# Kernel tuning notes

Hardware: AMD Instinct MI355X
Metric: run time of the kernel (lower is better)

Reference implementation:

```python
import jax, jax.numpy as jnp
import numpy as np
from jax import lax

B, T, H = 32768, 64, 16
VOCAB_USER = 600001
VOCAB_LAUNCH = 3


def setup_inputs() -> dict:
    key = jax.random.key(0)
    ks = jax.random.split(key, 10)
    s = 1.0 / np.sqrt(H)
    return {
        "user_id": jax.random.randint(ks[0], (B,), 0, VOCAB_USER),
        "launch_seq": jax.random.randint(ks[1], (B, T), 0, VOCAB_LAUNCH),
        "user_emb": jax.random.normal(ks[2], (VOCAB_USER, H), dtype=jnp.float32),
        "launch_emb": jax.random.normal(ks[3], (VOCAB_LAUNCH, H), dtype=jnp.float32),
        "W_ih": jax.random.uniform(ks[4], (3 * H, H), jnp.float32, -s, s),
        "W_hh": jax.random.uniform(ks[5], (3 * H, H), jnp.float32, -s, s),
        "b_ih": jax.random.uniform(ks[6], (3 * H,), jnp.float32, -s, s),
        "b_hh": jax.random.uniform(ks[7], (3 * H,), jnp.float32, -s, s),
        "fc_W": jax.random.uniform(ks[8], (1, 2 * H), jnp.float32, -s, s),
        "fc_b": jax.random.uniform(ks[9], (1,), jnp.float32, -s, s),
    }


def reference(user_id, launch_seq, user_emb, launch_emb, W_ih, W_hh, b_ih, b_hh, fc_W, fc_b):
    u = user_emb[user_id]                      # (B, H)
    x = launch_emb[launch_seq]                 # (B, T, H)
    # precompute input contributions to the gates for all timesteps
    gx_all = jnp.einsum('bth,gh->btg', x, W_ih) + b_ih  # (B, T, 3H)

    def step(h, gx):
        gh = h @ W_hh.T + b_hh                 # (B, 3H)
        r = jax.nn.sigmoid(gx[:, :H] + gh[:, :H])
        z = jax.nn.sigmoid(gx[:, H:2 * H] + gh[:, H:2 * H])
        n = jnp.tanh(gx[:, 2 * H:] + r * gh[:, 2 * H:])
        h_new = (1.0 - z) * n + z * h
        return h_new, h_new

    h0 = jnp.zeros((x.shape[0], H), dtype=x.dtype)
    _, hs = lax.scan(step, h0, jnp.swapaxes(gx_all, 0, 1))  # hs: (T, B, H)
    pooled = jnp.mean(hs, axis=0)              # (B, H)
    fc_in = jnp.concatenate([u, pooled], axis=1)  # (B, 2H)
    return fc_in @ fc_W.T + fc_b               # (B, 1)
```

## Files before the change

### kernel.cpp

```cpp
#include <hip/hip_runtime.h>
#include <hip/hip_bf16.h>
#include <string.h>


#define NBLK 1024

typedef __attribute__((ext_vector_type(8)))  short    short8;
typedef __attribute__((ext_vector_type(16))) float    floatx16;
typedef __attribute__((ext_vector_type(4)))  unsigned uintx4;

static __device__ __forceinline__ float fexp2(float x) { return __builtin_amdgcn_exp2f(x); }
static __device__ __forceinline__ float frcp(float x)  { return __builtin_amdgcn_rcpf(x); }
static __device__ __forceinline__ unsigned f2u(float f) { unsigned u; memcpy(&u, &f, 4); return u; }
static __device__ __forceinline__ unsigned short bfrne(float f) {
    union { __hip_bfloat16 b; unsigned short u; } cv; cv.b = __float2bfloat16(f); return cv.u;
}
static __device__ __forceinline__ float bf2f(unsigned short u) {
    unsigned v = ((unsigned)u) << 16; float f; memcpy(&f, &v, 4); return f;
}
static __device__ __forceinline__ unsigned pkrnd(float a, float b) {
    unsigned ua = f2u(a) + 0x8000u;
    unsigned ub = f2u(b) + 0x8000u;
    return __builtin_amdgcn_perm(ub, ua, 0x07060302u);
}
static __device__ __forceinline__ float sel3f(int c, float a0, float a1, float a2) {
    return c == 0 ? a0 : (c == 1 ? a1 : a2);
}
static __device__ __forceinline__ unsigned sel3u(int c, unsigned a0, unsigned a1, unsigned a2) {
    return c == 0 ? a0 : (c == 1 ? a1 : a2);
}

__global__ __launch_bounds__(64) void gru_mfma32(
    const int* __restrict__ user_id,
    const int* __restrict__ launch_seq,
    const float* __restrict__ user_emb,
    const float* __restrict__ launch_emb,
    const float* __restrict__ W_ih,
    const float* __restrict__ W_hh,
    const float* __restrict__ b_ih,
    const float* __restrict__ b_hh,
    const float* __restrict__ fc_W,
    const float* __restrict__ fc_b,
    float* __restrict__ out)
{
    constexpr float L  = 1.4426950408889634f;
    constexpr float L2 = 2.8853900817779268f;

    __shared__ float gxlut[144];

    const int tid  = threadIdx.x;
    const int n    = tid & 31;
    const int half = tid >> 5;
    const int d1o  = 4 * half;
    const long long sampBase = (long long)blockIdx.x * 32;

    unsigned pk[4];
    {
        const int* sp = launch_seq + (sampBase + n) * 64;
        #pragma unroll
        for (int w = 0; w < 4; ++w) {
            unsigned p = 0;
            #pragma unroll
            for (int j = 0; j < 4; ++j) {
                int4 v = ((const int4*)sp)[w * 4 + j];
                p |= ((unsigned)v.x & 3u) << (2 * (4 * j + 0));
                p |= ((unsigned)v.y & 3u) << (2 * (4 * j + 1));
                p |= ((unsigned)v.z & 3u) << (2 * (4 * j + 2));
                p |= ((unsigned)v.w & 3u) << (2 * (4 * j + 3));
            }
            pk[w] = p;
        }
    }

    for (int idx = tid; idx < 144; idx += 64) {
        int s = idx / 48, g = idx - s * 48;
        float dot = b_ih[g];
        #pragma unroll
        for (int k = 0; k < 16; ++k)
            dot = fmaf(W_ih[g * 16 + k], launch_emb[s * 16 + k], dot);
        int gate = g >> 4, dim = g & 15;
        gxlut[(gate * 3 + s) * 16 + dim] =
            (g < 32) ? (-L * (dot + b_hh[g])) : (L2 * dot);
    }

    short8 Arz, An;
    {
        auto pack8 = [&](const float* w) {
            uintx4 hi;
            #pragma unroll
            for (int p = 0; p < 4; ++p)
                hi[p] = (unsigned)bfrne(w[2 * p]) | ((unsigned)bfrne(w[2 * p + 1]) << 16);
            return __builtin_bit_cast(short8, hi);
        };
        float w[8];
        const float* rowrz = W_hh + n * 16;
        float4 a = *(const float4*)(rowrz + d1o);
        float4 b = *(const float4*)(rowrz + d1o + 8);
        w[0] = -L * a.x; w[1] = -L * a.y; w[2] = -L * a.z; w[3] = -L * a.w;
        w[4] = -L * b.x; w[5] = -L * b.y; w[6] = -L * b.z; w[7] = -L * b.w;
        Arz = pack8(w);
        if (n < 16) {
            const float* rown = W_hh + (32 + n) * 16;
            a = *(const float4*)(rown + d1o);
            b = *(const float4*)(rown + d1o + 8);
            w[0] = L2 * a.x; w[1] = L2 * a.y; w[2] = L2 * a.z; w[3] = L2 * a.w;
            w[4] = L2 * b.x; w[5] = L2 * b.y; w[6] = L2 * b.z; w[7] = L2 * b.w;
        } else {
            #pragma unroll
            for (int j = 0; j < 8; ++j) w[j] = 0.f;
        }
        An = pack8(w);
    }

    __syncthreads();

    short8 Agx;
    {
        uintx4 d = {0u, 0u, 0u, 0u};
        if (half == 0) {
            const float* base = (n < 16) ? &gxlut[0] : &gxlut[48];
            int dim = n & 15;
            float g0 = base[0 * 16 + dim];
            float g1 = base[1 * 16 + dim];
            float g2 = base[2 * 16 + dim];
            unsigned short h0 = bfrne(g0), h1 = bfrne(g1), h2 = bfrne(g2);
            d[0] = (unsigned)h0 | ((unsigned)h1 << 16);
            d[1] = (unsigned)h2 | ((unsigned)bfrne(g0 - bf2f(h0)) << 16);
            d[2] = (unsigned)bfrne(g1 - bf2f(h1)) | ((unsigned)bfrne(g2 - bf2f(h2)) << 16);
        }
        Agx = __builtin_bit_cast(short8, d);
    }

    const unsigned khA = half ? 0u : 0x3F80u;
    const unsigned khB = half ? 0u : 0x3F800000u;

    floatx16 Cn;
    #pragma unroll
    for (int i = 0; i < 16; ++i) Cn[i] = 0.f;
    {
        float4 a = *(const float4*)&b_hh[32 + d1o];
        float4 b = *(const float4*)&b_hh[32 + d1o + 8];
        Cn[0] = L2 * a.x; Cn[1] = L2 * a.y; Cn[2] = L2 * a.z; Cn[3] = L2 * a.w;
        Cn[4] = L2 * b.x; Cn[5] = L2 * b.y; Cn[6] = L2 * b.z; Cn[7] = L2 * b.w;
    }

    float gxn[3][8];
    #pragma unroll
    for (int c = 0; c < 3; ++c) {
        float4 a = *(const float4*)&gxlut[(6 + c) * 16 + d1o];
        float4 b = *(const float4*)&gxlut[(6 + c) * 16 + d1o + 8];
        gxn[c][0] = a.x; gxn[c][1] = a.y; gxn[c][2] = a.z; gxn[c][3] = a.w;
        gxn[c][4] = b.x; gxn[c][5] = b.y; gxn[c][6] = b.z; gxn[c][7] = b.w;
    }

    floatx16 CZ;
    #pragma unroll
    for (int i = 0; i < 16; ++i) CZ[i] = 0.f;

    float h[8], pool[8];
    #pragma unroll
    for (int j = 0; j < 8; ++j) { h[j] = 0.f; pool[j] = 0.f; }
    short8 B = {0, 0, 0, 0, 0, 0, 0, 0};

    short8 Bp;
    {
        int c0 = (int)(pk[0] & 3u);
        uintx4 bp = { sel3u(c0, khA, khB, 0u),
                      sel3u(c0, khB, 0u, khA),
                      sel3u(c0, 0u, khA, khB), 0u };
        Bp = __builtin_bit_cast(short8, bp);
    }

    #pragma unroll
    for (int w = 0; w < 4; ++w) {
        unsigned cw  = pk[w];
        unsigned ncw = (pk[w] >> 2) | (w < 3 ? (pk[w + 1] << 30) : 0u);
        #pragma unroll
        for (int tt = 0; tt < 16; ++tt) {
            int c = (int)(cw & 3u);

            floatx16 t1  = __builtin_amdgcn_mfma_f32_32x32x16_bf16(Agx, Bp, CZ, 0, 0, 0);
            floatx16 dn  = __builtin_amdgcn_mfma_f32_32x32x16_bf16(An,  B, Cn, 0, 0, 0);
            floatx16 drz = __builtin_amdgcn_mfma_f32_32x32x16_bf16(Arz, B, t1, 0, 0, 0);

            #pragma unroll
            for (int j = 0; j < 8; ++j) {
                float gn = sel3f(c, gxn[0][j], gxn[1][j], gxn[2][j]);
                float r  = frcp(1.0f + fexp2(drz[j]));
                float z  = frcp(1.0f + fexp2(drz[8 + j]));
                float y  = fmaf(r, dn[j], gn);
                float nn = fmaf(-2.0f, frcp(1.0f + fexp2(y)), 1.0f);
                h[j] = fmaf(z, h[j] - nn, nn);
                pool[j] += h[j];
            }

            int cn = (int)(ncw & 3u);
            uintx4 bp = { sel3u(cn, khA, khB, 0u),
                          sel3u(cn, khB, 0u, khA),
                          sel3u(cn, 0u, khA, khB), 0u };
            Bp = __builtin_bit_cast(short8, bp);
            uintx4 b;
            b[0] = pkrnd(h[0], h[1]);
            b[1] = pkrnd(h[2], h[3]);
            b[2] = pkrnd(h[4], h[5]);
            b[3] = pkrnd(h[6], h[7]);
            B = __builtin_bit_cast(short8, b);
            cw >>= 2;
            ncw >>= 2;
        }
    }

    float4 f1a = *(const float4*)&fc_W[d1o];
    float4 f1b = *(const float4*)&fc_W[d1o + 8];
    float4 f2a = *(const float4*)&fc_W[16 + d1o];
    float4 f2b = *(const float4*)&fc_W[16 + d1o + 8];
    int uid = user_id[sampBase + n];
    float4 ua = *(const float4*)&user_emb[(long long)uid * 16 + d1o];
    float4 ub = *(const float4*)&user_emb[(long long)uid * 16 + d1o + 8];
    const float inv64 = 1.0f / 64.0f;
    float val = f1a.x * ua.x + f1a.y * ua.y + f1a.z * ua.z + f1a.w * ua.w
              + f1b.x * ub.x + f1b.y * ub.y + f1b.z * ub.z + f1b.w * ub.w;
    val = fmaf(f2a.x * inv64, pool[0], val);
    val = fmaf(f2a.y * inv64, pool[1], val);
    val = fmaf(f2a.z * inv64, pool[2], val);
    val = fmaf(f2a.w * inv64, pool[3], val);
    val = fmaf(f2b.x * inv64, pool[4], val);
    val = fmaf(f2b.y * inv64, pool[5], val);
    val = fmaf(f2b.z * inv64, pool[6], val);
    val = fmaf(f2b.w * inv64, pool[7], val);
    val += __shfl_xor(val, 32);
    if (half == 0) out[sampBase + n] = val + fc_b[0];
}

extern "C" void kernel_launch(void* const* d_in, const int* in_sizes, int n_in,
                              void* d_out, int out_size, void* d_ws, size_t ws_size,
                              hipStream_t stream) {
    const int*   user_id    = (const int*)d_in[0];
    const int*   launch_seq = (const int*)d_in[1];
    const float* user_emb   = (const float*)d_in[2];
    const float* launch_emb = (const float*)d_in[3];
    const float* W_ih       = (const float*)d_in[4];
    const float* W_hh       = (const float*)d_in[5];
    const float* b_ih       = (const float*)d_in[6];
    const float* b_hh       = (const float*)d_in[7];
    const float* fc_W       = (const float*)d_in[8];
    const float* fc_b       = (const float*)d_in[9];
    float* out = (float*)d_out;

    gru_mfma32<<<dim3(NBLK), dim3(64), 0, stream>>>(
        user_id, launch_seq, user_emb, launch_emb,
        W_ih, W_hh, b_ih, b_hh, fc_W, fc_b, out);
}
```

Before: 126.6 us.

## Split GRU gate math across two cooperating waves with LDS hidden-state exchange

Each block now runs two wavefronts for the same 32 samples. Both waves issue the full MFMAs redundantly, but each computes the gate nonlinearities for only half of the hidden dimensions. The halves of the hidden state are exchanged through double-buffered shared memory with a barrier every timestep, and a final cross-wave reduction produces the output. The aim is to halve the serial transcendental work per wave on the recurrence critical path, at the cost of duplicated MFMAs, a block barrier per step, and a partial loop unroll.

```diff
diff --git a/kernel.cpp b/kernel.cpp
--- a/kernel.cpp
+++ b/kernel.cpp
@@ -30,7 +30,7 @@
     return c == 0 ? a0 : (c == 1 ? a1 : a2);
 }
 
-__global__ __launch_bounds__(64) void gru_mfma32(
+__global__ __launch_bounds__(128) void gru_coop(
     const int* __restrict__ user_id,
     const int* __restrict__ launch_seq,
     const float* __restrict__ user_emb,
@@ -46,12 +46,17 @@
     constexpr float L  = 1.4426950408889634f;
     constexpr float L2 = 2.8853900817779268f;
 
-    __shared__ float gxlut[144];
+    __shared__ float    gxlut[144];
+    __shared__ unsigned xch[2][2][64][2];
+    __shared__ float    redc[2][32];
 
     const int tid  = threadIdx.x;
-    const int n    = tid & 31;
-    const int half = tid >> 5;
+    const int wid  = tid >> 6;
+    const int lane = tid & 63;
+    const int n    = lane & 31;
+    const int half = lane >> 5;
     const int d1o  = 4 * half;
+    const int dimo = d1o + 8 * wid;
     const long long sampBase = (long long)blockIdx.x * 32;
 
     unsigned pk[4];
@@ -72,7 +77,7 @@
         }
     }
 
-    for (int idx = tid; idx < 144; idx += 64) {
+    for (int idx = tid; idx < 144; idx += 128) {
         int s = idx / 48, g = idx - s * 48;
         float dot = b_ih[g];
         #pragma unroll
@@ -144,22 +149,21 @@
         Cn[4] = L2 * b.x; Cn[5] = L2 * b.y; Cn[6] = L2 * b.z; Cn[7] = L2 * b.w;
     }
 
-    float gxn[3][8];
-    #pragma unroll
-    for (int c = 0; c < 3; ++c) {
-        float4 a = *(const float4*)&gxlut[(6 + c) * 16 + d1o];
-        float4 b = *(const float4*)&gxlut[(6 + c) * 16 + d1o + 8];
-        gxn[c][0] = a.x; gxn[c][1] = a.y; gxn[c][2] = a.z; gxn[c][3] = a.w;
-        gxn[c][4] = b.x; gxn[c][5] = b.y; gxn[c][6] = b.z; gxn[c][7] = b.w;
+    float gxn0[4], gxn1[4], gxn2[4];
+    #pragma unroll
+    for (int jj = 0; jj < 4; ++jj) {
+        gxn0[jj] = gxlut[(6 + 0) * 16 + dimo + jj];
+        gxn1[jj] = gxlut[(6 + 1) * 16 + dimo + jj];
+        gxn2[jj] = gxlut[(6 + 2) * 16 + dimo + jj];
     }
 
     floatx16 CZ;
     #pragma unroll
     for (int i = 0; i < 16; ++i) CZ[i] = 0.f;
 
-    float h[8], pool[8];
-    #pragma unroll
-    for (int j = 0; j < 8; ++j) { h[j] = 0.f; pool[j] = 0.f; }
+    float h4[4], pool4[4];
+    #pragma unroll
+    for (int jj = 0; jj < 4; ++jj) { h4[jj] = 0.f; pool4[jj] = 0.f; }
     short8 B = {0, 0, 0, 0, 0, 0, 0, 0};
 
     short8 Bp;
@@ -175,7 +179,7 @@
     for (int w = 0; w < 4; ++w) {
         unsigned cw  = pk[w];
         unsigned ncw = (pk[w] >> 2) | (w < 3 ? (pk[w + 1] << 30) : 0u);
-        #pragma unroll
+        #pragma unroll 2
         for (int tt = 0; tt < 16; ++tt) {
             int c = (int)(cw & 3u);
 
@@ -183,53 +187,61 @@
             floatx16 dn  = __builtin_amdgcn_mfma_f32_32x32x16_bf16(An,  B, Cn, 0, 0, 0);
             floatx16 drz = __builtin_amdgcn_mfma_f32_32x32x16_bf16(Arz, B, t1, 0, 0, 0);
 
-            #pragma unroll
-            for (int j = 0; j < 8; ++j) {
-                float gn = sel3f(c, gxn[0][j], gxn[1][j], gxn[2][j]);
-                float r  = frcp(1.0f + fexp2(drz[j]));
-                float z  = frcp(1.0f + fexp2(drz[8 + j]));
-                float y  = fmaf(r, dn[j], gn);
-                float nn = fmaf(-2.0f, frcp(1.0f + fexp2(y)), 1.0f);
-                h[j] = fmaf(z, h[j] - nn, nn);
-                pool[j] += h[j];
-            }
-
-            int cn = (int)(ncw & 3u);
-            uintx4 bp = { sel3u(cn, khA, khB, 0u),
-                          sel3u(cn, khB, 0u, khA),
-                          sel3u(cn, 0u, khA, khB), 0u };
+            auto gates = [&](int JO) {
+                #pragma unroll
+                for (int jj = 0; jj < 4; ++jj) {
+                    float gn = sel3f(c, gxn0[jj], gxn1[jj], gxn2[jj]);
+                    float r  = frcp(1.0f + fexp2(drz[JO + jj]));
+                    float z  = frcp(1.0f + fexp2(drz[8 + JO + jj]));
+                    float y  = fmaf(r, dn[JO + jj], gn);
+                    float nn = fmaf(-2.0f, frcp(1.0f + fexp2(y)), 1.0f);
+                    h4[jj] = fmaf(z, h4[jj] - nn, nn);
+                    pool4[jj] += h4[jj];
+                }
+            };
+            if (wid == 0) gates(0); else gates(4);
+
+            unsigned hp0 = pkrnd(h4[0], h4[1]);
+            unsigned hp1 = pkrnd(h4[2], h4[3]);
+            int buf = tt & 1;
+            xch[buf][wid][lane][0] = hp0;
+            xch[buf][wid][lane][1] = hp1;
+            __syncthreads();
+            unsigned tw0 = xch[buf][wid ^ 1][lane][0];
+            unsigned tw1 = xch[buf][wid ^ 1][lane][1];
+
+            uintx4 b;
+            b[0] = wid ? tw0 : hp0;
+            b[1] = wid ? tw1 : hp1;
+            b[2] = wid ? hp0 : tw0;
+            b[3] = wid ? hp1 : tw1;
+            B = __builtin_bit_cast(short8, b);
+
+            int cnx = (int)(ncw & 3u);
+            uintx4 bp = { sel3u(cnx, khA, khB, 0u),
+                          sel3u(cnx, khB, 0u, khA),
+                          sel3u(cnx, 0u, khA, khB), 0u };
             Bp = __builtin_bit_cast(short8, bp);
-            uintx4 b;
-            b[0] = pkrnd(h[0], h[1]);
-            b[1] = pkrnd(h[2], h[3]);
-            b[2] = pkrnd(h[4], h[5]);
-            b[3] = pkrnd(h[6], h[7]);
-            B = __builtin_bit_cast(short8, b);
             cw >>= 2;
             ncw >>= 2;
         }
     }
 
-    float4 f1a = *(const float4*)&fc_W[d1o];
-    float4 f1b = *(const float4*)&fc_W[d1o + 8];
-    float4 f2a = *(const float4*)&fc_W[16 + d1o];
-    float4 f2b = *(const float4*)&fc_W[16 + d1o + 8];
+    float4 f1 = *(const float4*)&fc_W[dimo];
+    float4 f2 = *(const float4*)&fc_W[16 + dimo];
     int uid = user_id[sampBase + n];
-    float4 ua = *(const float4*)&user_emb[(long long)uid * 16 + d1o];
-    float4 ub = *(const float4*)&user_emb[(long long)uid * 16 + d1o + 8];
+    float4 uu = *(const float4*)&user_emb[(long long)uid * 16 + dimo];
     const float inv64 = 1.0f / 64.0f;
-    float val = f1a.x * ua.x + f1a.y * ua.y + f1a.z * ua.z + f1a.w * ua.w
-              + f1b.x * ub.x + f1b.y * ub.y + f1b.z * ub.z + f1b.w * ub.w;
-    val = fmaf(f2a.x * inv64, pool[0], val);
-    val = fmaf(f2a.y * inv64, pool[1], val);
-    val = fmaf(f2a.z * inv64, pool[2], val);
-    val = fmaf(f2a.w * inv64, pool[3], val);
-    val = fmaf(f2b.x * inv64, pool[4], val);
-    val = fmaf(f2b.y * inv64, pool[5], val);
-    val = fmaf(f2b.z * inv64, pool[6], val);
-    val = fmaf(f2b.w * inv64, pool[7], val);
+    float val = f1.x * uu.x + f1.y * uu.y + f1.z * uu.z + f1.w * uu.w;
+    val = fmaf(f2.x * inv64, pool4[0], val);
+    val = fmaf(f2.y * inv64, pool4[1], val);
+    val = fmaf(f2.z * inv64, pool4[2], val);
+    val = fmaf(f2.w * inv64, pool4[3], val);
     val += __shfl_xor(val, 32);
-    if (half == 0) out[sampBase + n] = val + fc_b[0];
+    if (half == 0) redc[wid][n] = val;
+    __syncthreads();
+    if (wid == 0 && half == 0)
+        out[sampBase + n] = redc[0][n] + redc[1][n] + fc_b[0];
 }
 
 extern "C" void kernel_launch(void* const* d_in, const int* in_sizes, int n_in,
@@ -247,7 +259,7 @@
     const float* fc_b       = (const float*)d_in[9];
     float* out = (float*)d_out;
 
-    gru_mfma32<<<dim3(NBLK), dim3(64), 0, stream>>>(
+    gru_coop<<<dim3(NBLK), dim3(128), 0, stream>>>(
         user_id, launch_seq, user_emb, launch_emb,
         W_ih, W_hh, b_ih, b_hh, fc_W, fc_b, out);
 }
```

After: 233.6 us. 1.85x slower.

## Switch GRU recurrence to 16x16x32 MFMA with 16 samples per wave

Applied to the files above, without the earlier changes.

Restructures the recurrent step to use three 16x16x32 bf16 MFMAs (r, z, n gates), with 16 samples per 64-lane wave instead of 32, doubling the block count. The input-gate lookup and biases are folded into an extra K-slice (quad 2) of the B operand via one-hot rows, and the hidden state is redistributed across lanes with ds_bpermute each step. The sigmoid pair shares one reciprocal. The aim is a shorter per-step MFMA latency chain and more waves to hide it, at the cost of per-step cross-lane permutes and less work per wave.

```diff
diff --git a/kernel.cpp b/kernel.cpp
--- a/kernel.cpp
+++ b/kernel.cpp
@@ -3,11 +3,11 @@
 #include <string.h>
 
 
-#define NBLK 1024
-
-typedef __attribute__((ext_vector_type(8)))  short    short8;
-typedef __attribute__((ext_vector_type(16))) float    floatx16;
-typedef __attribute__((ext_vector_type(4)))  unsigned uintx4;
+#define NBLK 2048
+
+typedef __attribute__((ext_vector_type(8))) short    short8;
+typedef __attribute__((ext_vector_type(4))) float    floatx4;
+typedef __attribute__((ext_vector_type(4))) unsigned uintx4;
 
 static __device__ __forceinline__ float fexp2(float x) { return __builtin_amdgcn_exp2f(x); }
 static __device__ __forceinline__ float frcp(float x)  { return __builtin_amdgcn_rcpf(x); }
@@ -30,7 +30,7 @@
     return c == 0 ? a0 : (c == 1 ? a1 : a2);
 }
 
-__global__ __launch_bounds__(64) void gru_mfma32(
+__global__ __launch_bounds__(64) void gru16(
     const int* __restrict__ user_id,
     const int* __restrict__ launch_seq,
     const float* __restrict__ user_emb,
@@ -45,18 +45,20 @@
 {
     constexpr float L  = 1.4426950408889634f;
     constexpr float L2 = 2.8853900817779268f;
+    constexpr unsigned K_LO = 0x3F80u;
+    constexpr unsigned K_HI = 0x3F800000u;
 
     __shared__ float gxlut[144];
 
     const int tid  = threadIdx.x;
-    const int n    = tid & 31;
-    const int half = tid >> 5;
-    const int d1o  = 4 * half;
-    const long long sampBase = (long long)blockIdx.x * 32;
+    const int col  = tid & 15;
+    const int quad = tid >> 4;
+    const bool isq2 = (quad == 2);
+    const long long sampBase = (long long)blockIdx.x * 16;
 
     unsigned pk[4];
     {
-        const int* sp = launch_seq + (sampBase + n) * 64;
+        const int* sp = launch_seq + (sampBase + col) * 64;
         #pragma unroll
         for (int w = 0; w < 4; ++w) {
             unsigned p = 0;
@@ -83,7 +85,9 @@
             (g < 32) ? (-L * (dot + b_hh[g])) : (L2 * dot);
     }
 
-    short8 Arz, An;
+    __syncthreads();
+
+    short8 Ar, Az, An_;
     {
         auto pack8 = [&](const float* w) {
             uintx4 hi;
@@ -92,144 +96,122 @@
                 hi[p] = (unsigned)bfrne(w[2 * p]) | ((unsigned)bfrne(w[2 * p + 1]) << 16);
             return __builtin_bit_cast(short8, hi);
         };
-        float w[8];
-        const float* rowrz = W_hh + n * 16;
-        float4 a = *(const float4*)(rowrz + d1o);
-        float4 b = *(const float4*)(rowrz + d1o + 8);
-        w[0] = -L * a.x; w[1] = -L * a.y; w[2] = -L * a.z; w[3] = -L * a.w;
-        w[4] = -L * b.x; w[5] = -L * b.y; w[6] = -L * b.z; w[7] = -L * b.w;
-        Arz = pack8(w);
-        if (n < 16) {
-            const float* rown = W_hh + (32 + n) * 16;
-            a = *(const float4*)(rown + d1o);
-            b = *(const float4*)(rown + d1o + 8);
-            w[0] = L2 * a.x; w[1] = L2 * a.y; w[2] = L2 * a.z; w[3] = L2 * a.w;
-            w[4] = L2 * b.x; w[5] = L2 * b.y; w[6] = L2 * b.z; w[7] = L2 * b.w;
-        } else {
+        auto makeA = [&](int grow, float scale, const float* gx3, float bias, short8& A) {
+            float w[8];
             #pragma unroll
             for (int j = 0; j < 8; ++j) w[j] = 0.f;
-        }
-        An = pack8(w);
-    }
-
-    __syncthreads();
-
-    short8 Agx;
-    {
-        uintx4 d = {0u, 0u, 0u, 0u};
-        if (half == 0) {
-            const float* base = (n < 16) ? &gxlut[0] : &gxlut[48];
-            int dim = n & 15;
-            float g0 = base[0 * 16 + dim];
-            float g1 = base[1 * 16 + dim];
-            float g2 = base[2 * 16 + dim];
-            unsigned short h0 = bfrne(g0), h1 = bfrne(g1), h2 = bfrne(g2);
-            d[0] = (unsigned)h0 | ((unsigned)h1 << 16);
-            d[1] = (unsigned)h2 | ((unsigned)bfrne(g0 - bf2f(h0)) << 16);
-            d[2] = (unsigned)bfrne(g1 - bf2f(h1)) | ((unsigned)bfrne(g2 - bf2f(h2)) << 16);
-        }
-        Agx = __builtin_bit_cast(short8, d);
-    }
-
-    const unsigned khA = half ? 0u : 0x3F80u;
-    const unsigned khB = half ? 0u : 0x3F800000u;
-
-    floatx16 Cn;
-    #pragma unroll
-    for (int i = 0; i < 16; ++i) Cn[i] = 0.f;
-    {
-        float4 a = *(const float4*)&b_hh[32 + d1o];
-        float4 b = *(const float4*)&b_hh[32 + d1o + 8];
-        Cn[0] = L2 * a.x; Cn[1] = L2 * a.y; Cn[2] = L2 * a.z; Cn[3] = L2 * a.w;
-        Cn[4] = L2 * b.x; Cn[5] = L2 * b.y; Cn[6] = L2 * b.z; Cn[7] = L2 * b.w;
-    }
-
-    float gxn[3][8];
-    #pragma unroll
-    for (int c = 0; c < 3; ++c) {
-        float4 a = *(const float4*)&gxlut[(6 + c) * 16 + d1o];
-        float4 b = *(const float4*)&gxlut[(6 + c) * 16 + d1o + 8];
-        gxn[c][0] = a.x; gxn[c][1] = a.y; gxn[c][2] = a.z; gxn[c][3] = a.w;
-        gxn[c][4] = b.x; gxn[c][5] = b.y; gxn[c][6] = b.z; gxn[c][7] = b.w;
-    }
-
-    floatx16 CZ;
-    #pragma unroll
-    for (int i = 0; i < 16; ++i) CZ[i] = 0.f;
-
-    float h[8], pool[8];
-    #pragma unroll
-    for (int j = 0; j < 8; ++j) { h[j] = 0.f; pool[j] = 0.f; }
-    short8 B = {0, 0, 0, 0, 0, 0, 0, 0};
-
-    short8 Bp;
+            if (quad < 2) {
+                const float* row = W_hh + (grow + col) * 16 + quad * 8;
+                float4 a = *(const float4*)row;
+                float4 b = *(const float4*)(row + 4);
+                w[0] = scale * a.x; w[1] = scale * a.y; w[2] = scale * a.z; w[3] = scale * a.w;
+                w[4] = scale * b.x; w[5] = scale * b.y; w[6] = scale * b.z; w[7] = scale * b.w;
+            } else if (quad == 2) {
+                if (gx3) {
+                    #pragma unroll
+                    for (int c = 0; c < 3; ++c) {
+                        float g = gx3[c * 16 + col];
+                        w[c] = g;
+                        w[3 + c] = g - bf2f(bfrne(g));
+                    }
+                } else {
+                    w[6] = bias;
+                    w[7] = bias - bf2f(bfrne(bias));
+                }
+            }
+            A = pack8(w);
+        };
+        makeA(0,  -L, &gxlut[0],       0.f,               Ar);
+        makeA(16, -L, &gxlut[3 * 16],  0.f,               Az);
+        makeA(32,  L2, (const float*)0, L2 * b_hh[32 + col], An_);
+    }
+
+    floatx4 gn0 = *(const floatx4*)&gxlut[(6 + 0) * 16 + quad * 4];
+    floatx4 gn1 = *(const floatx4*)&gxlut[(6 + 1) * 16 + quad * 4];
+    floatx4 gn2 = *(const floatx4*)&gxlut[(6 + 2) * 16 + quad * 4];
+
+    const int a_lo = (col + 32 * (quad & 1)) * 4;
+    const int a_hi = a_lo + 64;
+
+    floatx4 h    = {0.f, 0.f, 0.f, 0.f};
+    floatx4 pool = {0.f, 0.f, 0.f, 0.f};
+    const floatx4 CZ = {0.f, 0.f, 0.f, 0.f};
+
+    short8 B;
     {
         int c0 = (int)(pk[0] & 3u);
-        uintx4 bp = { sel3u(c0, khA, khB, 0u),
-                      sel3u(c0, khB, 0u, khA),
-                      sel3u(c0, 0u, khA, khB), 0u };
-        Bp = __builtin_bit_cast(short8, bp);
+        uintx4 b = {0u, 0u, 0u, 0u};
+        if (isq2) {
+            b[0] = sel3u(c0, K_LO, K_HI, 0u);
+            b[1] = sel3u(c0, K_HI, 0u, K_LO);
+            b[2] = sel3u(c0, 0u, K_LO, K_HI);
+            b[3] = K_LO | K_HI;
+        }
+        B = __builtin_bit_cast(short8, b);
     }
 
     #pragma unroll
     for (int w = 0; w < 4; ++w) {
         unsigned cw  = pk[w];
         unsigned ncw = (pk[w] >> 2) | (w < 3 ? (pk[w + 1] << 30) : 0u);
-        #pragma unroll
+        #pragma unroll 4
         for (int tt = 0; tt < 16; ++tt) {
             int c = (int)(cw & 3u);
 
-            floatx16 t1  = __builtin_amdgcn_mfma_f32_32x32x16_bf16(Agx, Bp, CZ, 0, 0, 0);
-            floatx16 dn  = __builtin_amdgcn_mfma_f32_32x32x16_bf16(An,  B, Cn, 0, 0, 0);
-            floatx16 drz = __builtin_amdgcn_mfma_f32_32x32x16_bf16(Arz, B, t1, 0, 0, 0);
-
-            #pragma unroll
-            for (int j = 0; j < 8; ++j) {
-                float gn = sel3f(c, gxn[0][j], gxn[1][j], gxn[2][j]);
-                float r  = frcp(1.0f + fexp2(drz[j]));
-                float z  = frcp(1.0f + fexp2(drz[8 + j]));
-                float y  = fmaf(r, dn[j], gn);
+            floatx4 dr = __builtin_amdgcn_mfma_f32_16x16x32_bf16(Ar,  B, CZ, 0, 0, 0);
+            floatx4 dz = __builtin_amdgcn_mfma_f32_16x16x32_bf16(Az,  B, CZ, 0, 0, 0);
+            floatx4 dn = __builtin_amdgcn_mfma_f32_16x16x32_bf16(An_, B, CZ, 0, 0, 0);
+
+            #pragma unroll
+            for (int e = 0; e < 4; ++e) {
+                float er = fexp2(dr[e]);
+                float ez = fexp2(dz[e]);
+                float t1 = 1.0f + er;
+                float t2 = 1.0f + ez;
+                float rp = frcp(t1 * t2);
+                float r  = rp * t2;
+                float z  = rp * t1;
+                float gn = sel3f(c, gn0[e], gn1[e], gn2[e]);
+                float y  = fmaf(r, dn[e], gn);
                 float nn = fmaf(-2.0f, frcp(1.0f + fexp2(y)), 1.0f);
-                h[j] = fmaf(z, h[j] - nn, nn);
-                pool[j] += h[j];
+                h[e] = fmaf(z, h[e] - nn, nn);
+                pool[e] += h[e];
             }
 
+            unsigned hp0 = pkrnd(h[0], h[1]);
+            unsigned hp1 = pkrnd(h[2], h[3]);
             int cn = (int)(ncw & 3u);
-            uintx4 bp = { sel3u(cn, khA, khB, 0u),
-                          sel3u(cn, khB, 0u, khA),
-                          sel3u(cn, 0u, khA, khB), 0u };
-            Bp = __builtin_bit_cast(short8, bp);
             uintx4 b;
-            b[0] = pkrnd(h[0], h[1]);
-            b[1] = pkrnd(h[2], h[3]);
-            b[2] = pkrnd(h[4], h[5]);
-            b[3] = pkrnd(h[6], h[7]);
+            b[0] = (unsigned)__builtin_amdgcn_ds_bpermute(a_lo, (int)hp0);
+            b[1] = (unsigned)__builtin_amdgcn_ds_bpermute(a_lo, (int)hp1);
+            b[2] = (unsigned)__builtin_amdgcn_ds_bpermute(a_hi, (int)hp0);
+            b[3] = (unsigned)__builtin_amdgcn_ds_bpermute(a_hi, (int)hp1);
+            unsigned oh0 = sel3u(cn, K_LO, K_HI, 0u);
+            unsigned oh1 = sel3u(cn, K_HI, 0u, K_LO);
+            unsigned oh2 = sel3u(cn, 0u, K_LO, K_HI);
+            b[0] = isq2 ? oh0 : b[0];
+            b[1] = isq2 ? oh1 : b[1];
+            b[2] = isq2 ? oh2 : b[2];
+            b[3] = isq2 ? (K_LO | K_HI) : b[3];
             B = __builtin_bit_cast(short8, b);
             cw >>= 2;
             ncw >>= 2;
         }
     }
 
-    float4 f1a = *(const float4*)&fc_W[d1o];
-    float4 f1b = *(const float4*)&fc_W[d1o + 8];
-    float4 f2a = *(const float4*)&fc_W[16 + d1o];
-    float4 f2b = *(const float4*)&fc_W[16 + d1o + 8];
-    int uid = user_id[sampBase + n];
-    float4 ua = *(const float4*)&user_emb[(long long)uid * 16 + d1o];
-    float4 ub = *(const float4*)&user_emb[(long long)uid * 16 + d1o + 8];
+    float4 f1 = *(const float4*)&fc_W[quad * 4];
+    float4 f2 = *(const float4*)&fc_W[16 + quad * 4];
+    int uid = user_id[sampBase + col];
+    float4 uu = *(const float4*)&user_emb[(long long)uid * 16 + quad * 4];
     const float inv64 = 1.0f / 64.0f;
-    float val = f1a.x * ua.x + f1a.y * ua.y + f1a.z * ua.z + f1a.w * ua.w
-              + f1b.x * ub.x + f1b.y * ub.y + f1b.z * ub.z + f1b.w * ub.w;
-    val = fmaf(f2a.x * inv64, pool[0], val);
-    val = fmaf(f2a.y * inv64, pool[1], val);
-    val = fmaf(f2a.z * inv64, pool[2], val);
-    val = fmaf(f2a.w * inv64, pool[3], val);
-    val = fmaf(f2b.x * inv64, pool[4], val);
-    val = fmaf(f2b.y * inv64, pool[5], val);
-    val = fmaf(f2b.z * inv64, pool[6], val);
-    val = fmaf(f2b.w * inv64, pool[7], val);
+    float val = f1.x * uu.x + f1.y * uu.y + f1.z * uu.z + f1.w * uu.w;
+    val = fmaf(f2.x * inv64, pool[0], val);
+    val = fmaf(f2.y * inv64, pool[1], val);
+    val = fmaf(f2.z * inv64, pool[2], val);
+    val = fmaf(f2.w * inv64, pool[3], val);
+    val += __shfl_xor(val, 16);
     val += __shfl_xor(val, 32);
-    if (half == 0) out[sampBase + n] = val + fc_b[0];
+    if (quad == 0) out[sampBase + col] = val + fc_b[0];
 }
 
 extern "C" void kernel_launch(void* const* d_in, const int* in_sizes, int n_in,
@@ -247,7 +229,7 @@
     const float* fc_b       = (const float*)d_in[9];
     float* out = (float*)d_out;
 
-    gru_mfma32<<<dim3(NBLK), dim3(64), 0, stream>>>(
+    gru16<<<dim3(NBLK), dim3(64), 0, stream>>>(
         user_id, launch_seq, user_emb, launch_emb,
         W_ih, W_hh, b_ih, b_hh, fc_W, fc_b, out);
 }
```

New measurement: 133.7 us. +5.5%, slower.
